# Performance work log

Measured on AMD Instinct MI355X. Metric: run time of the kernel, lower is better.

## Reference

```python
import jax, jax.numpy as jnp
import numpy as np

POS_THRESHOLD = 0.5
B, N, A = 8, 262144, 64


def setup_inputs() -> dict:
    key = jax.random.key(0)
    k1, k2, k3 = jax.random.split(key, 3)
    # anchors: (y_center, x_center, h, w); centers in [0,1), positive h,w
    anchorss = jax.random.uniform(k1, (B, N, 4), dtype=jnp.float32)
    anchorss = anchorss.at[..., 2:].set(anchorss[..., 2:] * 0.3 + 0.01)  # h,w in (0.01, 0.31)
    # gt boxes as (y1, x1, y2, x2) with y1<y2, x1<x2
    raw = jax.random.uniform(k2, (B, A, 2, 2), dtype=jnp.float32)  # [...,coord_pair,(lo,hi)]
    lo = jnp.min(raw, axis=-1)  # (B,A,2) -> y1,x1
    hi = jnp.max(raw, axis=-1)  # (B,A,2) -> y2,x2
    gt_bboxess = jnp.concatenate([lo, hi], axis=-1)  # (B,A,4) = (y1,x1,y2,x2)
    gt_counts = jax.random.randint(k3, (B, 1), 1, A, dtype=jnp.int32)
    return {"anchorss": anchorss, "gt_bboxess": gt_bboxess,
            "gt_counts": gt_counts, "use_anchor": 1}


def reference(anchorss, gt_bboxess, gt_counts, use_anchor):
    # anchorss: (B,N,4), gt_bboxess: (B,A,4), gt_counts: (B,1)
    if use_anchor:
        y, x, h, w = (anchorss[..., i] for i in range(4))  # (B,N)
        y1 = y - h / 2
        y2 = y1 + h
        x1 = x - w / 2
        x2 = x1 + w
        area = h * w
    else:
        y1, x1, y2, x2 = (anchorss[..., i] for i in range(4))
        area = (y2 - y1) * (x2 - x1)
    gy1, gx1, gy2, gx2 = (gt_bboxess[..., i] for i in range(4))  # (B,A)
    ga = (gy2 - gy1) * (gx2 - gx1)  # (B,A)
    # broadcast anchors (B,N,1) against gts (B,1,A): same clamp math as torch
    yy1 = jnp.clip(y1[:, :, None], gy1[:, None, :], gy2[:, None, :])
    xx1 = jnp.clip(x1[:, :, None], gx1[:, None, :], gx2[:, None, :])
    yy2 = jnp.clip(y2[:, :, None], gy1[:, None, :], gy2[:, None, :])
    xx2 = jnp.clip(x2[:, :, None], gx1[:, None, :], gx2[:, None, :])
    inter = (yy2 - yy1) * (xx2 - xx1)  # (B,N,A)
    union = area[:, :, None] + ga[:, None, :] - inter
    iou = inter / union
    # mask out invalid gts (index >= gt_count per batch)
    valid = jnp.arange(A, dtype=gt_counts.dtype)[None, :] < gt_counts  # (B,A)
    pos = (iou >= POS_THRESHOLD) & valid[:, None, :]  # (B,N,A)
    labels = jnp.any(pos, axis=2).astype(jnp.int32)[..., None]  # (B,N,1)
    return labels
```

## Files before the change

kernel.cpp:

```cpp
#include <hip/hip_runtime.h>

typedef float f32x2 __attribute__((ext_vector_type(2)));

constexpr int BLOCK = 512;
constexpr int IPT   = 2;
constexpr int BPB   = 8;
constexpr int PAD   = 8;

__global__ __launch_bounds__(BLOCK, 2) void assign_cls_label_kernel(
    const float* __restrict__ anchorss,
    const float* __restrict__ gt_bboxess,
    const int* __restrict__ gt_counts,
    const int* __restrict__ use_anchor_p,
    int* __restrict__ out,
    int N, int A, int B)
{
#pragma clang fp contract(off)
    extern __shared__ float4 s_box[];
    __shared__ int s_count[BPB];

    const int AS  = A + PAD;
    const int tid = threadIdx.x;
    const int b0  = blockIdx.y * BPB;
    const int nbA = ((B - b0 < BPB) ? (B - b0) : BPB) * A;

    const int n0r = blockIdx.x * (BLOCK * IPT) + tid;
    const int n1r = n0r + BLOCK;
    const int n0  = (n0r < N) ? n0r : N - 1;
    const int n1  = (n1r < N) ? n1r : N - 1;

    float4 an0 = ((const float4*)anchorss)[(size_t)b0 * N + n0];
    float4 an1 = ((const float4*)anchorss)[(size_t)b0 * N + n1];

    for (int i = tid; i < nbA; i += BLOCK) {
        const int bb = i / A, gi = i - bb * A;
        s_box[bb * AS + gi] = ((const float4*)gt_bboxess)[(size_t)(b0 + bb) * A + gi];
    }
    if (tid < BPB) s_count[tid] = (b0 + tid < B) ? gt_counts[b0 + tid] : 0;

    const int use_anchor = use_anchor_p[0];
    __syncthreads();

    const float c26 = 1.0f / 67108864.0f;

#pragma clang loop unroll(disable)
    for (int bb = 0; bb < BPB; ++bb) {
        if (b0 + bb >= B) break;
        const float4 ac0 = an0, ac1 = an1;
        if (bb + 1 < BPB && b0 + bb + 1 < B) {
            const float4* arow = (const float4*)anchorss + (size_t)(b0 + bb + 1) * N;
            an0 = arow[n0];
            an1 = arow[n1];
        }

        f32x2 Y1, X1, Y2, X2, AREA;
        if (use_anchor) {
            const f32x2 H  = {ac0.z, ac1.z};
            const f32x2 W  = {ac0.w, ac1.w};
            const f32x2 Yc = {ac0.x, ac1.x};
            const f32x2 Xc = {ac0.y, ac1.y};
            Y1 = Yc - H * 0.5f;
            Y2 = Y1 + H;
            X1 = Xc - W * 0.5f;
            X2 = X1 + W;
            AREA = H * W;
        } else {
            Y1 = f32x2{ac0.x, ac1.x}; X1 = f32x2{ac0.y, ac1.y};
            Y2 = f32x2{ac0.z, ac1.z}; X2 = f32x2{ac0.w, ac1.w};
            AREA = (Y2 - Y1) * (X2 - X1);
        }
        f32x2 ACC = {-1.0f, -1.0f};

        const float4* sb    = s_box + bb * AS;
        const int     count = s_count[bb];

        auto comp = [&](const float4 g) {
            const float ga = (g.z - g.x) * (g.w - g.y);
            f32x2 yy1, yy2, xx1, xx2;
            yy1.x = __builtin_amdgcn_fmed3f(Y1.x, g.x, g.z);
            yy1.y = __builtin_amdgcn_fmed3f(Y1.y, g.x, g.z);
            yy2.x = __builtin_amdgcn_fmed3f(Y2.x, g.x, g.z);
            yy2.y = __builtin_amdgcn_fmed3f(Y2.y, g.x, g.z);
            xx1.x = __builtin_amdgcn_fmed3f(X1.x, g.y, g.w);
            xx1.y = __builtin_amdgcn_fmed3f(X1.y, g.y, g.w);
            xx2.x = __builtin_amdgcn_fmed3f(X2.x, g.y, g.w);
            xx2.y = __builtin_amdgcn_fmed3f(X2.y, g.y, g.w);
            const f32x2 dy    = yy2 - yy1;
            const f32x2 dx    = xx2 - xx1;
            const f32x2 inter = dy * dx;
            const f32x2 u     = (AREA + ga) - inter;
            const f32x2 mh    = {-0.5f, -0.5f};
            const f32x2 cc    = {c26, c26};
            const f32x2 e = __builtin_elementwise_fma(u, mh, inter);
            const f32x2 r = __builtin_elementwise_fma(u, cc, e);
            ACC = __builtin_elementwise_max(ACC, r);
        };

        float4 gA0, gA1, gA2, gA3, gB0, gB1, gB2, gB3;
        gA0 = sb[0]; gA1 = sb[1]; gA2 = sb[2]; gA3 = sb[3];
        int gi = 0;
        while (gi + 8 <= count) {
            gB0 = sb[gi + 4]; gB1 = sb[gi + 5]; gB2 = sb[gi + 6]; gB3 = sb[gi + 7];
            comp(gA0); comp(gA1); comp(gA2); comp(gA3);
            gA0 = sb[gi + 8]; gA1 = sb[gi + 9]; gA2 = sb[gi + 10]; gA3 = sb[gi + 11];
            comp(gB0); comp(gB1); comp(gB2); comp(gB3);
            gi += 8;
        }
        const int rem = count - gi;
        if (rem > 4) { gB0 = sb[gi + 4]; gB1 = sb[gi + 5]; gB2 = sb[gi + 6]; gB3 = sb[gi + 7]; }
        if (rem > 0) comp(gA0);
        if (rem > 1) comp(gA1);
        if (rem > 2) comp(gA2);
        if (rem > 3) comp(gA3);
        if (rem > 4) comp(gB0);
        if (rem > 5) comp(gB1);
        if (rem > 6) comp(gB2);

        int* orow = out + (size_t)(b0 + bb) * N;
        if (n0r < N) orow[n0r] = (ACC.x >= 0.0f) ? 1 : 0;
        if (n1r < N) orow[n1r] = (ACC.y >= 0.0f) ? 1 : 0;
    }
}

extern "C" void kernel_launch(void* const* d_in, const int* in_sizes, int n_in,
                              void* d_out, int out_size, void* d_ws, size_t ws_size,
                              hipStream_t stream) {
    const float* anchorss   = (const float*)d_in[0];
    const float* gt_bboxess = (const float*)d_in[1];
    const int*   gt_counts  = (const int*)d_in[2];
    const int*   use_anchor = (const int*)d_in[3];
    int*         out        = (int*)d_out;

    const int B = in_sizes[2];
    const int A = in_sizes[1] / (4 * B);
    const int N = in_sizes[0] / (4 * B);

    dim3 grid((N + BLOCK * IPT - 1) / (BLOCK * IPT), (B + BPB - 1) / BPB);
    size_t smem = (size_t)(BPB * (A + PAD)) * sizeof(float4);
    hipLaunchKernelGGL(assign_cls_label_kernel, grid, dim3(BLOCK), smem, stream,
                       anchorss, gt_bboxess, gt_counts, use_anchor, out, N, A, B);
}
```

Baseline: 95.78 us.

## Read GT boxes directly from global memory instead of staging in LDS

Removes the shared-memory staging of ground-truth boxes and the block barrier, and loads boxes and counts straight from global memory. Inside the loop the box addresses are wave-uniform, so the compiler may emit scalar loads, and the prefetch indices are clamped to stay in bounds. Block size is halved to 256, which doubles the grid and shortens each block's lifetime. The cost is more cache traffic per box, and scalar-load latency may not be hidden as well as LDS reads were.

```diff
diff --git a/kernel.cpp b/kernel.cpp
--- a/kernel.cpp
+++ b/kernel.cpp
@@ -2,27 +2,21 @@
 
 typedef float f32x2 __attribute__((ext_vector_type(2)));
 
-constexpr int BLOCK = 512;
+constexpr int BLOCK = 256;
 constexpr int IPT   = 2;
 constexpr int BPB   = 8;
-constexpr int PAD   = 8;
 
 __global__ __launch_bounds__(BLOCK, 2) void assign_cls_label_kernel(
     const float* __restrict__ anchorss,
-    const float* __restrict__ gt_bboxess,
+    const float4* __restrict__ gt_boxes4,
     const int* __restrict__ gt_counts,
     const int* __restrict__ use_anchor_p,
     int* __restrict__ out,
     int N, int A, int B)
 {
 #pragma clang fp contract(off)
-    extern __shared__ float4 s_box[];
-    __shared__ int s_count[BPB];
-
-    const int AS  = A + PAD;
     const int tid = threadIdx.x;
     const int b0  = blockIdx.y * BPB;
-    const int nbA = ((B - b0 < BPB) ? (B - b0) : BPB) * A;
 
     const int n0r = blockIdx.x * (BLOCK * IPT) + tid;
     const int n1r = n0r + BLOCK;
@@ -32,20 +26,16 @@
     float4 an0 = ((const float4*)anchorss)[(size_t)b0 * N + n0];
     float4 an1 = ((const float4*)anchorss)[(size_t)b0 * N + n1];
 
-    for (int i = tid; i < nbA; i += BLOCK) {
-        const int bb = i / A, gi = i - bb * A;
-        s_box[bb * AS + gi] = ((const float4*)gt_bboxess)[(size_t)(b0 + bb) * A + gi];
-    }
-    if (tid < BPB) s_count[tid] = (b0 + tid < B) ? gt_counts[b0 + tid] : 0;
-
-    const int use_anchor = use_anchor_p[0];
-    __syncthreads();
-
+    const int   use_anchor = use_anchor_p[0];
     const float c26 = 1.0f / 67108864.0f;
+    const int   Am1 = A - 1;
 
 #pragma clang loop unroll(disable)
     for (int bb = 0; bb < BPB; ++bb) {
         if (b0 + bb >= B) break;
+        const int count = gt_counts[b0 + bb];
+        const float4* __restrict__ grow = gt_boxes4 + (size_t)(b0 + bb) * A;
+
         const float4 ac0 = an0, ac1 = an1;
         if (bb + 1 < BPB && b0 + bb + 1 < B) {
             const float4* arow = (const float4*)anchorss + (size_t)(b0 + bb + 1) * N;
@@ -71,9 +61,6 @@
         }
         f32x2 ACC = {-1.0f, -1.0f};
 
-        const float4* sb    = s_box + bb * AS;
-        const int     count = s_count[bb];
-
         auto comp = [&](const float4 g) {
             const float ga = (g.z - g.x) * (g.w - g.y);
             f32x2 yy1, yy2, xx1, xx2;
@@ -96,25 +83,33 @@
             ACC = __builtin_elementwise_max(ACC, r);
         };
 
-        float4 gA0, gA1, gA2, gA3, gB0, gB1, gB2, gB3;
-        gA0 = sb[0]; gA1 = sb[1]; gA2 = sb[2]; gA3 = sb[3];
+        float4 g0, g1, g2, g3, h0, h1, h2, h3;
+        g0 = grow[0];
+        g1 = grow[min(1, Am1)];
+        g2 = grow[min(2, Am1)];
+        g3 = grow[min(3, Am1)];
         int gi = 0;
         while (gi + 8 <= count) {
-            gB0 = sb[gi + 4]; gB1 = sb[gi + 5]; gB2 = sb[gi + 6]; gB3 = sb[gi + 7];
-            comp(gA0); comp(gA1); comp(gA2); comp(gA3);
-            gA0 = sb[gi + 8]; gA1 = sb[gi + 9]; gA2 = sb[gi + 10]; gA3 = sb[gi + 11];
-            comp(gB0); comp(gB1); comp(gB2); comp(gB3);
+            h0 = grow[gi + 4]; h1 = grow[gi + 5];
+            h2 = grow[gi + 6]; h3 = grow[gi + 7];
+            comp(g0); comp(g1); comp(g2); comp(g3);
+            g0 = grow[min(gi + 8,  Am1)]; g1 = grow[min(gi + 9,  Am1)];
+            g2 = grow[min(gi + 10, Am1)]; g3 = grow[min(gi + 11, Am1)];
+            comp(h0); comp(h1); comp(h2); comp(h3);
             gi += 8;
         }
         const int rem = count - gi;
-        if (rem > 4) { gB0 = sb[gi + 4]; gB1 = sb[gi + 5]; gB2 = sb[gi + 6]; gB3 = sb[gi + 7]; }
-        if (rem > 0) comp(gA0);
-        if (rem > 1) comp(gA1);
-        if (rem > 2) comp(gA2);
-        if (rem > 3) comp(gA3);
-        if (rem > 4) comp(gB0);
-        if (rem > 5) comp(gB1);
-        if (rem > 6) comp(gB2);
+        if (rem > 4) {
+            h0 = grow[min(gi + 4, Am1)]; h1 = grow[min(gi + 5, Am1)];
+            h2 = grow[min(gi + 6, Am1)]; h3 = grow[min(gi + 7, Am1)];
+        }
+        if (rem > 0) comp(g0);
+        if (rem > 1) comp(g1);
+        if (rem > 2) comp(g2);
+        if (rem > 3) comp(g3);
+        if (rem > 4) comp(h0);
+        if (rem > 5) comp(h1);
+        if (rem > 6) comp(h2);
 
         int* orow = out + (size_t)(b0 + bb) * N;
         if (n0r < N) orow[n0r] = (ACC.x >= 0.0f) ? 1 : 0;
@@ -125,18 +120,17 @@
 extern "C" void kernel_launch(void* const* d_in, const int* in_sizes, int n_in,
                               void* d_out, int out_size, void* d_ws, size_t ws_size,
                               hipStream_t stream) {
-    const float* anchorss   = (const float*)d_in[0];
-    const float* gt_bboxess = (const float*)d_in[1];
-    const int*   gt_counts  = (const int*)d_in[2];
-    const int*   use_anchor = (const int*)d_in[3];
-    int*         out        = (int*)d_out;
+    const float*  anchorss   = (const float*)d_in[0];
+    const float4* gt_boxes4  = (const float4*)d_in[1];
+    const int*    gt_counts  = (const int*)d_in[2];
+    const int*    use_anchor = (const int*)d_in[3];
+    int*          out        = (int*)d_out;
 
     const int B = in_sizes[2];
     const int A = in_sizes[1] / (4 * B);
     const int N = in_sizes[0] / (4 * B);
 
     dim3 grid((N + BLOCK * IPT - 1) / (BLOCK * IPT), (B + BPB - 1) / BPB);
-    size_t smem = (size_t)(BPB * (A + PAD)) * sizeof(float4);
-    hipLaunchKernelGGL(assign_cls_label_kernel, grid, dim3(BLOCK), smem, stream,
-                       anchorss, gt_bboxess, gt_counts, use_anchor, out, N, A, B);
+    hipLaunchKernelGGL(assign_cls_label_kernel, grid, dim3(BLOCK), 0, stream,
+                       anchorss, gt_boxes4, gt_counts, use_anchor, out, N, A, B);
 }
```

Result: slower. 99.58 us (+4.0%).
